# Kernel optimization log

Hardware: AMD Instinct MI355X
Metric: run time of the kernel (lower is better)

The kernel has to match this reference:

```python
import jax, jax.numpy as jnp
import numpy as np

N_NODES = 100000
N_EDGES = 1600000
F_IN = 16
F_OUT = 16
N_BASIS = 4  # per spatial dim; basisTerms = [4, 4]


def linear_basis(u, n):
    """Piecewise-linear (hat) basis, n terms on [-1, 1]. u: [E] -> [E, n]."""
    centers = jnp.linspace(-1.0, 1.0, n, dtype=u.dtype)
    dx = 2.0 / (n - 1)
    return jnp.maximum(0.0, 1.0 - jnp.abs(u[:, None] - centers[None, :]) / dx)


def setup_inputs() -> dict:
    key = jax.random.key(0)
    k1, k2, k3, k4, k5 = jax.random.split(key, 5)
    x = jax.random.normal(k1, (N_NODES, F_IN), dtype=jnp.float32)
    edge_index = jax.random.randint(k2, (2, N_EDGES), 0, N_NODES, dtype=jnp.int64)
    # relative positions normalized to [-1, 1]^2 (as in initializeWeights2D)
    edge_attr = jax.random.uniform(k3, (N_EDGES, 2), dtype=jnp.float32,
                                   minval=-1.0, maxval=1.0)
    # weight: [*basisTerms, inputFeatures, outputFeatures], uniform(-0.05, 0.05)
    weight = jax.random.uniform(k4, (N_BASIS, N_BASIS, F_IN, F_OUT),
                                dtype=jnp.float32, minval=-0.05, maxval=0.05)
    return {"x": x, "edge_index": edge_index, "edge_attr": edge_attr,
            "weight": weight}


def reference(x, edge_index, edge_attr, weight):
    """BasisConvLayer forward, mode='conv', linear basis, no bias/activations.

    For each edge e=(i<-j): msg_e = sum_{u,v} b_u(dx) b_v(dy) * (x_j @ W[u,v]);
    out[i] = sum over incoming edges of msg_e.
    """
    row, col = edge_index[0], edge_index[1]
    x_j = x[col]                                   # [E, F_in] gather
    bx = linear_basis(edge_attr[:, 0], N_BASIS)    # [E, nB]
    by = linear_basis(edge_attr[:, 1], N_BASIS)    # [E, nB]
    # outer product of 1D bases -> [E, nB*nB] interpolation coefficients
    t = (bx[:, :, None] * by[:, None, :]).reshape(-1, N_BASIS * N_BASIS)
    w_flat = weight.reshape(N_BASIS * N_BASIS, F_IN, F_OUT)
    # accumulate over the small fixed basis-term set to avoid [E, Fin, Fout]
    msg = jnp.zeros((x_j.shape[0], F_OUT), dtype=x.dtype)
    for k in range(N_BASIS * N_BASIS):
        msg = msg + t[:, k, None] * (x_j @ w_flat[k])
    out = jax.ops.segment_sum(msg, row, num_segments=N_NODES)  # scatter-add
    return out
```

## Files before the change

kernel.cpp:

```cpp
#include <hip/hip_runtime.h>
#include <hip/hip_fp16.h>

#define N_NODES 100000
#define N_EDGES 1600000
#define Y_ELEMS ((size_t)N_NODES * 256)
#define Y_BYTES (Y_ELEMS * 2)
#define ACC_ELEMS ((size_t)N_NODES * 16)
#define ACC_BYTES (ACC_ELEMS * 2)
#define WS_NEEDED (Y_BYTES + ACC_BYTES)

__global__ __launch_bounds__(256) void zero_acc_kernel(uint4* __restrict__ p, int n) {
    int i = blockIdx.x * 256 + threadIdx.x;
    if (i < n) p[i] = make_uint4(0, 0, 0, 0);
}

#define XROW 20
__global__ __launch_bounds__(256) void stage1_xw_f16(
    const float* __restrict__ x,
    const float* __restrict__ w,
    unsigned short* __restrict__ Y)
{
    __shared__ float xls[4 * 64 * XROW];
    const int lane = threadIdx.x & 63;
    const int wid  = threadIdx.x >> 6;
    const int k  = lane >> 2;
    const int fq = lane & 3;
    const int batch = blockIdx.x * 4 + wid;
    const int base  = batch * 64;
    if (base >= N_NODES) return;

    float4 wr[16];
#pragma unroll
    for (int i = 0; i < 16; ++i)
        wr[i] = *(const float4*)(w + k * 256 + i * 16 + fq * 4);

    float* xl = &xls[wid * 64 * XROW];
    const int nl = base + lane;
    if (nl < N_NODES) {
        const float4* xr = (const float4*)(x + (size_t)nl * 16);
#pragma unroll
        for (int q = 0; q < 4; ++q)
            *(float4*)(xl + lane * XROW + q * 4) = xr[q];
    }
    __builtin_amdgcn_s_waitcnt(0);

    const int nmax = (N_NODES - base < 64) ? (N_NODES - base) : 64;
    for (int j = 0; j < nmax; ++j) {
        float xs[16];
#pragma unroll
        for (int q = 0; q < 4; ++q) {
            float4 t4 = *(const float4*)(xl + j * XROW + q * 4);
            xs[4*q+0] = t4.x; xs[4*q+1] = t4.y; xs[4*q+2] = t4.z; xs[4*q+3] = t4.w;
        }
        float4 acc = make_float4(0.f, 0.f, 0.f, 0.f);
#pragma unroll
        for (int i = 0; i < 16; ++i) {
            acc.x += xs[i] * wr[i].x; acc.y += xs[i] * wr[i].y;
            acc.z += xs[i] * wr[i].z; acc.w += xs[i] * wr[i].w;
        }
        __half2 h0 = __floats2half2_rn(acc.x, acc.y);
        __half2 h1 = __floats2half2_rn(acc.z, acc.w);
        unsigned int u0 = *(unsigned int*)&h0;
        unsigned int u1 = *(unsigned int*)&h1;
        uint2 o = make_uint2(u0, u1);
        *(uint2*)(Y + (size_t)(base + j) * 256 + k * 16 + fq * 4) = o;
    }
}

__global__ __launch_bounds__(256) void stage2_pk(
    const int*   __restrict__ edge_index,
    const float* __restrict__ edge_attr,
    const unsigned short* __restrict__ Y,
    __half2*     __restrict__ acc)
{
    const int g = blockIdx.x * 256 + threadIdx.x;
    const int e = g >> 3;
    const int l = g & 7;

    const int row = edge_index[e];
    const int col = edge_index[N_EDGES + e];
    const float2 attr = ((const float2*)edge_attr)[e];

    float fu = (attr.x + 1.0f) * 1.5f;
    int iu = (int)fu; iu = iu < 0 ? 0 : (iu > 2 ? 2 : iu);
    const float wu1 = fu - (float)iu;
    const float wu0 = 1.0f - wu1;

    float fv = (attr.y + 1.0f) * 1.5f;
    int iv = (int)fv; iv = iv < 0 ? 0 : (iv > 2 ? 2 : iv);
    const float wv1 = fv - (float)iv;
    const float wv0 = 1.0f - wv1;

    const float t00 = wu0 * wv0, t01 = wu0 * wv1;
    const float t10 = wu1 * wv0, t11 = wu1 * wv1;
    const int k0 = iu * 4 + iv;

    const __half2* yb = (const __half2*)(Y + (size_t)col * 256) + l;
    const float2 f00 = __half22float2(yb[(k0)     * 8]);
    const float2 f01 = __half22float2(yb[(k0 + 1) * 8]);
    const float2 f10 = __half22float2(yb[(k0 + 4) * 8]);
    const float2 f11 = __half22float2(yb[(k0 + 5) * 8]);

    const float m0 = t00 * f00.x + t01 * f01.x + t10 * f10.x + t11 * f11.x;
    const float m1 = t00 * f00.y + t01 * f01.y + t10 * f10.y + t11 * f11.y;

    unsafeAtomicAdd(acc + (size_t)row * 8 + l, __floats2half2_rn(m0, m1));
}

__global__ __launch_bounds__(256) void convert_kernel(
    const __half2* __restrict__ acc, float2* __restrict__ out, int n2) {
    int i = blockIdx.x * 256 + threadIdx.x;
    if (i < n2) out[i] = __half22float2(acc[i]);
}

__global__ __launch_bounds__(256) void zero_out_kernel(float4* __restrict__ out, int n4) {
    int i = blockIdx.x * 256 + threadIdx.x;
    if (i < n4) out[i] = make_float4(0.f, 0.f, 0.f, 0.f);
}
#define FSLAB 260
__global__ __launch_bounds__(256) void basis_conv_edges(
    const float* __restrict__ x, const int* __restrict__ edge_index,
    const float* __restrict__ edge_attr, const float* __restrict__ weight,
    float* __restrict__ out)
{
    __shared__ float wl[16 * FSLAB];
    for (int idx = threadIdx.x; idx < 4096; idx += 256) {
        const int f = idx & 15, i = (idx >> 4) & 15, k = idx >> 8;
        wl[f * FSLAB + k * 16 + i] = weight[idx];
    }
    __syncthreads();
    const int f = threadIdx.x & 15, s = threadIdx.x >> 4;
    const int ebase = blockIdx.x * 256;
#pragma unroll 1
    for (int it = 0; it < 16; ++it) {
        const int e = ebase + it * 16 + s;
        const int row = edge_index[e];
        const int col = edge_index[N_EDGES + e];
        const float2 attr = ((const float2*)edge_attr)[e];
        float fu = (attr.x + 1.0f) * 1.5f;
        int iu = (int)fu; iu = iu < 0 ? 0 : (iu > 2 ? 2 : iu);
        const float wu1 = fu - (float)iu, wu0 = 1.0f - wu1;
        float fv = (attr.y + 1.0f) * 1.5f;
        int iv = (int)fv; iv = iv < 0 ? 0 : (iv > 2 ? 2 : iv);
        const float wv1 = fv - (float)iv, wv0 = 1.0f - wv1;
        const int k0 = iu * 4 + iv;
        int kb[4] = {k0, k0 + 1, k0 + 4, k0 + 5};
        float tw[4] = {wu0 * wv0, wu0 * wv1, wu1 * wv0, wu1 * wv1};
        const float4* xv = (const float4*)(x + (size_t)col * 16);
        float xs[16];
#pragma unroll
        for (int q = 0; q < 4; ++q) {
            float4 t4 = xv[q];
            xs[4*q+0]=t4.x; xs[4*q+1]=t4.y; xs[4*q+2]=t4.z; xs[4*q+3]=t4.w;
        }
        float msg = 0.0f;
#pragma unroll
        for (int p = 0; p < 4; ++p) {
            const float t = tw[p];
            const float4* wp = (const float4*)&wl[f * FSLAB + kb[p] * 16];
#pragma unroll
            for (int i4 = 0; i4 < 4; ++i4) {
                const float4 w = wp[i4];
                msg += t * (xs[4*i4+0]*w.x + xs[4*i4+1]*w.y + xs[4*i4+2]*w.z + xs[4*i4+3]*w.w);
            }
        }
        unsafeAtomicAdd(out + (size_t)row * 16 + f, msg);
    }
}

extern "C" void kernel_launch(void* const* d_in, const int* in_sizes, int n_in,
                              void* d_out, int out_size, void* d_ws, size_t ws_size,
                              hipStream_t stream) {
    const float* x  = (const float*)d_in[0];
    const int*   ei = (const int*)d_in[1];
    const float* ea = (const float*)d_in[2];
    const float* w  = (const float*)d_in[3];
    float* out = (float*)d_out;

    if (ws_size >= WS_NEEDED) {
        unsigned short* Y = (unsigned short*)d_ws;
        __half2* acc = (__half2*)((char*)d_ws + Y_BYTES);

        const int nacc16 = (int)(ACC_BYTES / 16);
        zero_acc_kernel<<<(nacc16 + 255) / 256, 256, 0, stream>>>((uint4*)acc, nacc16);

        const int batches = (N_NODES + 63) / 64;
        stage1_xw_f16<<<(batches + 3) / 4, 256, 0, stream>>>(x, w, Y);

        stage2_pk<<<(N_EDGES * 8) / 256, 256, 0, stream>>>(ei, ea, Y, acc);

        const int n2 = (int)ACC_ELEMS / 2;
        convert_kernel<<<(n2 + 255) / 256, 256, 0, stream>>>(acc, (float2*)out, n2);
    } else {
        const int n4 = out_size / 4;
        zero_out_kernel<<<(n4 + 255) / 256, 256, 0, stream>>>((float4*)out, n4);
        basis_conv_edges<<<N_EDGES / 256, 256, 0, stream>>>(x, ei, ea, w, out);
    }
}
```

Before: 182.5 us.

## Store adjacent basis pairs contiguously in Y so each edge reads two rows

Stage 1 now writes each node's x@W products in a duplicated layout where basis terms (iu,iv) and (iu,iv+1) sit next to each other in 64-byte chunks, so stage 2 needs two contiguous loads per edge instead of four scattered ones. Stage 2 uses 16 lanes per edge, exchanges the pair halves with a cross-lane shuffle, and only the low 8 lanes do the atomic add. Stage 1 also moves from 64-node to 16-node batches per wave. The cost is a 1.5x larger Y buffer (more stage-1 write traffic) and twice as many stage-2 threads, half of which sit idle at the atomic.

```diff
diff --git a/kernel.cpp b/kernel.cpp
--- a/kernel.cpp
+++ b/kernel.cpp
@@ -3,53 +3,49 @@
 
 #define N_NODES 100000
 #define N_EDGES 1600000
-#define Y_ELEMS ((size_t)N_NODES * 256)
-#define Y_BYTES (Y_ELEMS * 2)
+#define Y2_HALFS_PER_NODE 384
+#define Y2_BYTES ((size_t)N_NODES * Y2_HALFS_PER_NODE * 2)
 #define ACC_ELEMS ((size_t)N_NODES * 16)
 #define ACC_BYTES (ACC_ELEMS * 2)
-#define WS_NEEDED (Y_BYTES + ACC_BYTES)
+#define WS_NEEDED (Y2_BYTES + ACC_BYTES)
 
 __global__ __launch_bounds__(256) void zero_acc_kernel(uint4* __restrict__ p, int n) {
     int i = blockIdx.x * 256 + threadIdx.x;
     if (i < n) p[i] = make_uint4(0, 0, 0, 0);
 }
 
-#define XROW 20
-__global__ __launch_bounds__(256) void stage1_xw_f16(
+__global__ __launch_bounds__(256) void stage1_xw_pair(
     const float* __restrict__ x,
     const float* __restrict__ w,
-    unsigned short* __restrict__ Y)
+    unsigned short* __restrict__ Y2)
 {
-    __shared__ float xls[4 * 64 * XROW];
+    __shared__ float4 xls[4][64];
     const int lane = threadIdx.x & 63;
     const int wid  = threadIdx.x >> 6;
     const int k  = lane >> 2;
     const int fq = lane & 3;
+    const int ku = k >> 2, kv = k & 3;
     const int batch = blockIdx.x * 4 + wid;
-    const int base  = batch * 64;
-    if (base >= N_NODES) return;
+    if (batch >= N_NODES / 16) return;
+    const int base = batch * 16;
 
     float4 wr[16];
 #pragma unroll
     for (int i = 0; i < 16; ++i)
         wr[i] = *(const float4*)(w + k * 256 + i * 16 + fq * 4);
 
-    float* xl = &xls[wid * 64 * XROW];
-    const int nl = base + lane;
-    if (nl < N_NODES) {
-        const float4* xr = (const float4*)(x + (size_t)nl * 16);
-#pragma unroll
-        for (int q = 0; q < 4; ++q)
-            *(float4*)(xl + lane * XROW + q * 4) = xr[q];
-    }
+    xls[wid][lane] = ((const float4*)(x + (size_t)base * 16))[lane];
     __builtin_amdgcn_s_waitcnt(0);
 
-    const int nmax = (N_NODES - base < 64) ? (N_NODES - base) : 64;
-    for (int j = 0; j < nmax; ++j) {
+    const int off_lo = (ku * 3 + kv) * 32 + fq * 4;
+    const int off_hi = (ku * 3 + (kv - 1)) * 32 + 16 + fq * 4;
+
+#pragma unroll 1
+    for (int j = 0; j < 16; ++j) {
         float xs[16];
 #pragma unroll
         for (int q = 0; q < 4; ++q) {
-            float4 t4 = *(const float4*)(xl + j * XROW + q * 4);
+            float4 t4 = xls[wid][j * 4 + q];
             xs[4*q+0] = t4.x; xs[4*q+1] = t4.y; xs[4*q+2] = t4.z; xs[4*q+3] = t4.w;
         }
         float4 acc = make_float4(0.f, 0.f, 0.f, 0.f);
@@ -60,22 +56,22 @@
         }
         __half2 h0 = __floats2half2_rn(acc.x, acc.y);
         __half2 h1 = __floats2half2_rn(acc.z, acc.w);
-        unsigned int u0 = *(unsigned int*)&h0;
-        unsigned int u1 = *(unsigned int*)&h1;
-        uint2 o = make_uint2(u0, u1);
-        *(uint2*)(Y + (size_t)(base + j) * 256 + k * 16 + fq * 4) = o;
-    }
-}
-
-__global__ __launch_bounds__(256) void stage2_pk(
+        uint2 o = make_uint2(*(unsigned int*)&h0, *(unsigned int*)&h1);
+        unsigned short* yrow = Y2 + (size_t)(base + j) * Y2_HALFS_PER_NODE;
+        if (kv <= 2) *(uint2*)(yrow + off_lo) = o;
+        if (kv >= 1) *(uint2*)(yrow + off_hi) = o;
+    }
+}
+
+__global__ __launch_bounds__(256) void stage2_pair(
     const int*   __restrict__ edge_index,
     const float* __restrict__ edge_attr,
-    const unsigned short* __restrict__ Y,
+    const unsigned short* __restrict__ Y2,
     __half2*     __restrict__ acc)
 {
     const int g = blockIdx.x * 256 + threadIdx.x;
-    const int e = g >> 3;
-    const int l = g & 7;
+    const int e = g >> 4;
+    const int l = g & 15;
 
     const int row = edge_index[e];
     const int col = edge_index[N_EDGES + e];
@@ -93,18 +89,27 @@
 
     const float t00 = wu0 * wv0, t01 = wu0 * wv1;
     const float t10 = wu1 * wv0, t11 = wu1 * wv1;
-    const int k0 = iu * 4 + iv;
-
-    const __half2* yb = (const __half2*)(Y + (size_t)col * 256) + l;
-    const float2 f00 = __half22float2(yb[(k0)     * 8]);
-    const float2 f01 = __half22float2(yb[(k0 + 1) * 8]);
-    const float2 f10 = __half22float2(yb[(k0 + 4) * 8]);
-    const float2 f11 = __half22float2(yb[(k0 + 5) * 8]);
-
-    const float m0 = t00 * f00.x + t01 * f01.x + t10 * f10.x + t11 * f11.x;
-    const float m1 = t00 * f00.y + t01 * f01.y + t10 * f10.y + t11 * f11.y;
-
-    unsafeAtomicAdd(acc + (size_t)row * 8 + l, __floats2half2_rn(m0, m1));
+
+    const unsigned int* yrow = (const unsigned int*)(Y2 + (size_t)col * Y2_HALFS_PER_NODE);
+    const unsigned int uA = yrow[(iu       * 3 + iv) * 16 + l];
+    const unsigned int uB = yrow[((iu + 1) * 3 + iv) * 16 + l];
+    const unsigned int uA2 = __shfl_xor((int)uA, 8);
+    const unsigned int uB2 = __shfl_xor((int)uB, 8);
+
+    const bool lowhalf = (l < 8);
+    const float tAo = lowhalf ? t00 : t01, tAp = lowhalf ? t01 : t00;
+    const float tBo = lowhalf ? t10 : t11, tBp = lowhalf ? t11 : t10;
+
+    const float2 fAo = __half22float2(*(const __half2*)&uA);
+    const float2 fAp = __half22float2(*(const __half2*)&uA2);
+    const float2 fBo = __half22float2(*(const __half2*)&uB);
+    const float2 fBp = __half22float2(*(const __half2*)&uB2);
+
+    const float m0 = tAo * fAo.x + tAp * fAp.x + tBo * fBo.x + tBp * fBp.x;
+    const float m1 = tAo * fAo.y + tAp * fAp.y + tBo * fBo.y + tBp * fBp.y;
+
+    if (lowhalf)
+        unsafeAtomicAdd(acc + (size_t)row * 8 + l, __floats2half2_rn(m0, m1));
 }
 
 __global__ __launch_bounds__(256) void convert_kernel(
@@ -178,16 +183,16 @@
     float* out = (float*)d_out;
 
     if (ws_size >= WS_NEEDED) {
-        unsigned short* Y = (unsigned short*)d_ws;
-        __half2* acc = (__half2*)((char*)d_ws + Y_BYTES);
+        unsigned short* Y2 = (unsigned short*)d_ws;
+        __half2* acc = (__half2*)((char*)d_ws + Y2_BYTES);
 
         const int nacc16 = (int)(ACC_BYTES / 16);
         zero_acc_kernel<<<(nacc16 + 255) / 256, 256, 0, stream>>>((uint4*)acc, nacc16);
 
-        const int batches = (N_NODES + 63) / 64;
-        stage1_xw_f16<<<(batches + 3) / 4, 256, 0, stream>>>(x, w, Y);
-
-        stage2_pk<<<(N_EDGES * 8) / 256, 256, 0, stream>>>(ei, ea, Y, acc);
+        const int batches = N_NODES / 16;
+        stage1_xw_pair<<<(batches + 3) / 4, 256, 0, stream>>>(x, w, Y2);
+
+        stage2_pair<<<(N_EDGES * 16) / 256, 256, 0, stream>>>(ei, ea, Y2, acc);
 
         const int n2 = (int)ACC_ELEMS / 2;
         convert_kernel<<<(n2 + 255) / 256, 256, 0, stream>>>(acc, (float2*)out, n2);
```

Result: slower. 188.4 us (+3.3%).
